# Kernel optimization log

Measured on AMD Instinct MI355X. Metric: run time of the kernel, lower is better.

The kernel has to match this reference:

```python
import jax, jax.numpy as jnp
import numpy as np

B, C, L = 8, 512, 2048
D = C // 8  # qk projection dim


def setup_inputs() -> dict:
    key = jax.random.key(0)
    ks = jax.random.split(key, 7)
    s = 0.02
    return {
        "x": jax.random.normal(ks[0], (B, C, L), dtype=jnp.float32),
        "data_mask": jnp.zeros((B, L, L), dtype=bool),
        "Wq": jax.random.normal(ks[1], (D, C), dtype=jnp.float32) * s,
        "bq": jnp.zeros((D,), dtype=jnp.float32),
        "Wk": jax.random.normal(ks[2], (D, C), dtype=jnp.float32) * s,
        "bk": jnp.zeros((D,), dtype=jnp.float32),
        "Wv": jax.random.normal(ks[3], (C, C), dtype=jnp.float32) * s,
        "bv": jnp.zeros((C,), dtype=jnp.float32),
    }


def reference(x, data_mask, Wq, bq, Wk, bk, Wv, bv):
    # Conv1d(kernel_size=1) == pointwise linear over channel dim.
    Lx = x.shape[-1]
    q = jnp.einsum("dc,bcl->bld", Wq, x) + bq              # (B, L, D)  == query_conv(x).permute(0,2,1)
    k = jnp.einsum("dc,bcl->bdl", Wk, x) + bk[:, None]     # (B, D, L)
    energy = jnp.einsum("bld,bdm->blm", q, k)              # (B, L, L)
    causal = jnp.triu(jnp.ones((Lx, Lx), dtype=bool), k=1)  # strictly-upper = masked
    mask = causal[None, :, :] | data_mask
    energy = jnp.where(mask, -jnp.inf, energy)
    attention = jax.nn.softmax(energy, axis=-1)            # (B, L, L)
    v = jnp.einsum("oc,bcl->bol", Wv, x) + bv[:, None]     # (B, C, L)
    # out = bmm(proj_value, attention^T): out[b,c,m] = sum_l v[b,c,l] * attention[b,m,l]
    out = jnp.einsum("bcl,bml->bcm", v, attention)         # (B, C, L)
    return out, attention
```

## Files before the change

### kernel.cpp

```cpp
#include <hip/hip_runtime.h>
#include <cstddef>
#include <math.h>

#define B_ 8
#define C_ 512
#define L_ 2048
#define D_ 64

typedef __bf16 bf16x8 __attribute__((ext_vector_type(8)));
typedef __bf16 bf16x4 __attribute__((ext_vector_type(4)));
typedef float f32x4 __attribute__((ext_vector_type(4)));

#define MFMA16 __builtin_amdgcn_mfma_f32_16x16x32_bf16

__device__ __forceinline__ void async_lds16(const void* g, void* l) {
  __builtin_amdgcn_global_load_lds(
      (const __attribute__((address_space(1))) void*)g,
      (__attribute__((address_space(3))) void*)l, 16, 0, 0);
}

__global__ __launch_bounds__(256) void transpose_cvt(const float* __restrict__ x,
                                                     __bf16* __restrict__ xT) {
  __shared__ float ts[64][68];
  const int b = blockIdx.z;
  const int l0 = blockIdx.x * 64, c0 = blockIdx.y * 64;
  const int t = threadIdx.x;
  const float* xb = x + ((size_t)b * C_ + c0) * L_ + l0;
#pragma unroll
  for (int kq = 0; kq < 4; ++kq) {
    const int i = t + kq * 256;
    const int row = i >> 4, col4 = i & 15;
    const float4 v = *(const float4*)(xb + (size_t)row * L_ + col4 * 4);
    *(f32x4*)&ts[row][col4 * 4] = *(const f32x4*)&v;
  }
  __syncthreads();
  __bf16* xTb = xT + ((size_t)b * L_ + l0) * C_ + c0;
  const int l = t >> 2, cq = (t & 3) * 16;
  bf16x8 o0, o1;
#pragma unroll
  for (int j = 0; j < 8; ++j) o0[j] = (__bf16)ts[cq + j][l];
#pragma unroll
  for (int j = 0; j < 8; ++j) o1[j] = (__bf16)ts[cq + 8 + j][l];
  *(bf16x8*)(xTb + (size_t)l * C_ + cq) = o0;
  *(bf16x8*)(xTb + (size_t)l * C_ + cq + 8) = o1;
}

__global__ __launch_bounds__(256) void prep_qkv(
    const float* __restrict__ Wq, const float* __restrict__ Wk,
    const float* __restrict__ Wv, const float* __restrict__ bq,
    const float* __restrict__ bk, const float* __restrict__ bv,
    __bf16* __restrict__ W, float* __restrict__ bias) {
  const int i = blockIdx.x * 256 + threadIdx.x;
  const int rq = 64 * 512 / 4;
  const int rk = 128 * 512 / 4;
  const float* src;
  int j;
  if (i < rq) {
    src = Wq; j = i;
  } else if (i < rk) {
    src = Wk; j = i - rq;
  } else {
    src = Wv; j = i - rk;
  }
  float4 v = ((const float4*)src)[j];
  bf16x4 h = {(__bf16)v.x, (__bf16)v.y, (__bf16)v.z, (__bf16)v.w};
  ((bf16x4*)W)[i] = h;
  if (blockIdx.x == 0) {
    for (int t = threadIdx.x; t < 640; t += 256)
      bias[t] = t < 64 ? bq[t] : (t < 128 ? bk[t - 64] : bv[t - 128]);
  }
}

__global__ __launch_bounds__(256) void gemm_qkv(
    const __bf16* __restrict__ A, const __bf16* __restrict__ Bm,
    const float* __restrict__ bias, __bf16* __restrict__ qh,
    __bf16* __restrict__ kh, __bf16* __restrict__ vh) {
  __shared__ __align__(16) __bf16 Ash[128 * 32];
  __shared__ __align__(16) __bf16 Bsh[128 * 32];
  const int b = blockIdx.z;
  const int m0 = blockIdx.x * 128;
  const int n0 = blockIdx.y * 128;
  const int tid = threadIdx.x;
  const int w = tid >> 6, lane = tid & 63;
  const int wm = (w & 1) * 64, wn = (w >> 1) * 64;
  const int lm = lane & 15, q8 = lane >> 4;
  const int srow = lane >> 2;
  const int sk8 = (lane & 3) ^ ((lane >> 3) & 3);

  const __bf16* Bb = Bm + (size_t)b * L_ * C_;
  f32x4 acc[4][4] = {};

  for (int k0 = 0; k0 < C_; k0 += 32) {
#pragma unroll
    for (int t = 0; t < 2; ++t) {
      const int rb = (t * 4 + w) * 16;
      async_lds16(A + (size_t)(m0 + rb + srow) * C_ + k0 + sk8 * 8,
                  &Ash[rb * 32]);
      async_lds16(Bb + (size_t)(n0 + rb + srow) * C_ + k0 + sk8 * 8,
                  &Bsh[rb * 32]);
    }
    __syncthreads();
    const int swz = (q8 ^ ((lm >> 1) & 3)) * 8;
    bf16x8 afr[4], bfr[4];
#pragma unroll
    for (int i = 0; i < 4; ++i) {
      afr[i] = *(const bf16x8*)&Ash[(wm + i * 16 + lm) * 32 + swz];
      bfr[i] = *(const bf16x8*)&Bsh[(wn + i * 16 + lm) * 32 + swz];
    }
#pragma unroll
    for (int i = 0; i < 4; ++i)
#pragma unroll
      for (int j = 0; j < 4; ++j)
        acc[i][j] = MFMA16(afr[i], bfr[j], acc[i][j], 0, 0, 0);
    __syncthreads();
  }

#pragma unroll
  for (int i = 0; i < 4; ++i) {
#pragma unroll
    for (int j = 0; j < 4; ++j) {
      const int ng = n0 + wn + j * 16 + lm;
      const int mg = m0 + wm + i * 16 + q8 * 4;
      if (mg < 128) {
        bf16x4 h;
#pragma unroll
        for (int r = 0; r < 4; ++r) h[r] = (__bf16)(acc[i][j][r] + bias[mg + r]);
        if (mg < 64)
          *(bf16x4*)&qh[((size_t)b * L_ + ng) * 64 + mg] = h;
        else
          *(bf16x4*)&kh[((size_t)b * L_ + ng) * 64 + mg - 64] = h;
      } else {
#pragma unroll
        for (int r = 0; r < 4; ++r)
          vh[((size_t)b * C_ + mg - 128 + r) * L_ + ng] =
              (__bf16)(acc[i][j][r] + bias[mg + r]);
      }
    }
  }
}

__global__ __launch_bounds__(256) void row_sums(
    const __bf16* __restrict__ q, const __bf16* __restrict__ k,
    const unsigned char* __restrict__ mask, float* __restrict__ sinv) {
  __shared__ __align__(16) __bf16 qs[32 * 64];
  __shared__ __align__(16) __bf16 ks[2][128 * 64];
  __shared__ __align__(16) unsigned char msk[2][32 * 128];
  __shared__ float sums[4][32];
  const int b = blockIdx.y;
  const int s = (b < 4) ? (int)blockIdx.x : 63 - (int)blockIdx.x;
  const int r0 = s * 32;
  const int T = (r0 + 31) / 128 + 1;
  const int tid = threadIdx.x;
  const int w = tid >> 6, lane = tid & 63;
  const int lm = lane & 15, q8 = lane >> 4;
  const __bf16* qb = q + (size_t)b * L_ * D_;
  const __bf16* kb = k + (size_t)b * L_ * D_;
  const int krow = lane >> 3;
  const int kk8 = (lane & 7) ^ ((lane >> 3) & 7);

  async_lds16(qb + (size_t)r0 * D_ + tid * 8, &qs[w * 512]);
#pragma unroll
  for (int r = 0; r < 4; ++r)
    async_lds16(kb + (size_t)(r * 32 + w * 8 + krow) * 64 + kk8 * 8,
                &ks[0][(r * 32 + w * 8) * 64]);
  async_lds16(mask + ((size_t)b * L_ + r0 + w * 8 + krow) * L_ + (lane & 7) * 16,
              &msk[0][w * 1024]);

  bf16x8 af[2][2];
  float rsum[2][4] = {};
  for (int t = 0; t < T; ++t) {
    const int t0 = t * 128, buf = t & 1;
    __syncthreads();
    if (t == 0) {
#pragma unroll
      for (int i = 0; i < 2; ++i)
#pragma unroll
        for (int kk = 0; kk < 2; ++kk)
          af[i][kk] = *(const bf16x8*)&qs[(i * 16 + lm) * 64 + kk * 32 + q8 * 8];
    }
    if (t + 1 < T) {
      const int nt0 = t0 + 128, nb = (t + 1) & 1;
#pragma unroll
      for (int r = 0; r < 4; ++r)
        async_lds16(kb + (size_t)(nt0 + r * 32 + w * 8 + krow) * 64 + kk8 * 8,
                    &ks[nb][(r * 32 + w * 8) * 64]);
      async_lds16(mask + ((size_t)b * L_ + r0 + w * 8 + krow) * L_ + nt0 +
                      (lane & 7) * 16,
                  &msk[nb][w * 1024]);
    }
    f32x4 acc[2][2] = {};
#pragma unroll
    for (int kk = 0; kk < 2; ++kk) {
#pragma unroll
      for (int j = 0; j < 2; ++j) {
        const int n = w * 32 + j * 16 + lm;
        const int k8i = kk * 4 + q8;
        bf16x8 bf = *(const bf16x8*)&ks[buf][n * 64 + ((k8i ^ (n & 7)) * 8)];
#pragma unroll
        for (int i = 0; i < 2; ++i)
          acc[i][j] = MFMA16(af[i][kk], bf, acc[i][j], 0, 0, 0);
      }
    }
#pragma unroll
    for (int i = 0; i < 2; ++i)
#pragma unroll
      for (int j = 0; j < 2; ++j)
#pragma unroll
        for (int r = 0; r < 4; ++r) {
          const int lr = i * 16 + q8 * 4 + r;
          const int mcol = w * 32 + j * 16 + lm;
          const int l = r0 + lr, m = t0 + mcol;
          const bool ok = (m <= l) && (msk[buf][lr * 128 + mcol] == 0);
          rsum[i][r] += ok ? __expf(acc[i][j][r]) : 0.f;
        }
  }
#pragma unroll
  for (int i = 0; i < 2; ++i)
#pragma unroll
    for (int r = 0; r < 4; ++r) {
      float vv = rsum[i][r];
      vv += __shfl_xor(vv, 1);
      vv += __shfl_xor(vv, 2);
      vv += __shfl_xor(vv, 4);
      vv += __shfl_xor(vv, 8);
      if (lm == 0) sums[w][i * 16 + q8 * 4 + r] = vv;
    }
  __syncthreads();
  if (tid < 32)
    sinv[(size_t)b * L_ + r0 + tid] =
        1.f / (sums[0][tid] + sums[1][tid] + sums[2][tid] + sums[3][tid]);
}

__global__ __launch_bounds__(256) void attn_fused(
    const __bf16* __restrict__ q, const __bf16* __restrict__ k,
    const __bf16* __restrict__ v, const unsigned char* __restrict__ mask,
    const float* __restrict__ sinv, float* __restrict__ att,
    float* __restrict__ out) {
  __shared__ __align__(16) __bf16 qs[32 * 64];
  __shared__ __align__(16) __bf16 ks[2][128 * 64];
  __shared__ __align__(16) unsigned char msk[2][32 * 128];
  __shared__ __align__(16) __bf16 Ps[32 * 136];
  const int gid = blockIdx.x;
  const int b = gid & 7;
  const int s0 = gid >> 3;
  const int s = (s0 < 32) ? s0 : 95 - s0;
  const int r0 = s * 32;
  const int T = (r0 + 31) / 128 + 1;
  const int tid = threadIdx.x;
  const int w = tid >> 6, lane = tid & 63;
  const int lm = lane & 15, q8 = lane >> 4;
  const __bf16* qb = q + (size_t)b * L_ * D_;
  const __bf16* kb = k + (size_t)b * L_ * D_;
  const __bf16* vb = v + (size_t)b * C_ * L_;
  const int krow = lane >> 3;
  const int kk8 = (lane & 7) ^ ((lane >> 3) & 7);

  float inv[2][4];
#pragma unroll
  for (int i = 0; i < 2; ++i)
#pragma unroll
    for (int r = 0; r < 4; ++r)
      inv[i][r] = sinv[(size_t)b * L_ + r0 + i * 16 + q8 * 4 + r];

  bf16x8 af[2][2];
  f32x4 accO[2][8] = {};

  async_lds16(qb + (size_t)r0 * D_ + tid * 8, &qs[w * 512]);
#pragma unroll
  for (int r = 0; r < 4; ++r)
    async_lds16(kb + (size_t)(r * 32 + w * 8 + krow) * 64 + kk8 * 8,
                &ks[0][(r * 32 + w * 8) * 64]);
  async_lds16(mask + ((size_t)b * L_ + r0 + w * 8 + krow) * L_ + (lane & 7) * 16,
              &msk[0][w * 1024]);

  for (int t = 0; t < T; ++t) {
    const int t0 = t * 128, buf = t & 1;
    __syncthreads();
    if (t == 0) {
#pragma unroll
      for (int i = 0; i < 2; ++i)
#pragma unroll
        for (int kk = 0; kk < 2; ++kk)
          af[i][kk] = *(const bf16x8*)&qs[(i * 16 + lm) * 64 + kk * 32 + q8 * 8];
    }
    if (t + 1 < T) {
      const int nt0 = t0 + 128, nb = (t + 1) & 1;
#pragma unroll
      for (int r = 0; r < 4; ++r)
        async_lds16(kb + (size_t)(nt0 + r * 32 + w * 8 + krow) * 64 + kk8 * 8,
                    &ks[nb][(r * 32 + w * 8) * 64]);
      async_lds16(mask + ((size_t)b * L_ + r0 + w * 8 + krow) * L_ + nt0 +
                      (lane & 7) * 16,
                  &msk[nb][w * 1024]);
    }
    f32x4 acc[2][2] = {};
#pragma unroll
    for (int kk = 0; kk < 2; ++kk) {
#pragma unroll
      for (int j = 0; j < 2; ++j) {
        const int n = w * 32 + j * 16 + lm;
        const int k8i = kk * 4 + q8;
        bf16x8 bf = *(const bf16x8*)&ks[buf][n * 64 + ((k8i ^ (n & 7)) * 8)];
#pragma unroll
        for (int i = 0; i < 2; ++i)
          acc[i][j] = MFMA16(af[i][kk], bf, acc[i][j], 0, 0, 0);
      }
    }
#pragma unroll
    for (int i = 0; i < 2; ++i)
#pragma unroll
      for (int j = 0; j < 2; ++j)
#pragma unroll
        for (int r = 0; r < 4; ++r) {
          const int lr = i * 16 + q8 * 4 + r;
          const int mcol = w * 32 + j * 16 + lm;
          const int l = r0 + lr, m = t0 + mcol;
          const bool ok = (m <= l) && (msk[buf][lr * 128 + mcol] == 0);
          const float p = ok ? __expf(acc[i][j][r]) : 0.f;
          att[((size_t)b * L_ + l) * L_ + m] = p * inv[i][r];
          Ps[lr * 136 + mcol] = (__bf16)p;
        }
    asm volatile("s_waitcnt lgkmcnt(0)\n\ts_barrier" ::: "memory");
    __builtin_amdgcn_sched_barrier(0);
#pragma unroll
    for (int kk = 0; kk < 4; ++kk) {
      bf16x8 pa[2];
#pragma unroll
      for (int i = 0; i < 2; ++i)
        pa[i] = *(const bf16x8*)&Ps[(i * 16 + lm) * 136 + kk * 32 + q8 * 8];
#pragma unroll
      for (int cf = 0; cf < 8; ++cf) {
        const int c = w * 128 + cf * 16 + lm;
        bf16x8 bv =
            *(const bf16x8*)(vb + (size_t)c * L_ + t0 + kk * 32 + q8 * 8);
#pragma unroll
        for (int i = 0; i < 2; ++i)
          accO[i][cf] = MFMA16(pa[i], bv, accO[i][cf], 0, 0, 0);
      }
    }
  }

#pragma unroll
  for (int i = 0; i < 2; ++i)
#pragma unroll
    for (int cf = 0; cf < 8; ++cf) {
      const int c = w * 128 + cf * 16 + lm;
      f32x4 o;
      o[0] = accO[i][cf][0] * inv[i][0];
      o[1] = accO[i][cf][1] * inv[i][1];
      o[2] = accO[i][cf][2] * inv[i][2];
      o[3] = accO[i][cf][3] * inv[i][3];
      *(f32x4*)(out + ((size_t)b * C_ + c) * L_ + r0 + i * 16 + q8 * 4) = o;
    }

  const f32x4 z4 = {0.f, 0.f, 0.f, 0.f};
  for (int rr = 0; rr < 32; ++rr) {
    float* arow = att + ((size_t)b * L_ + r0 + rr) * L_;
    for (int c = T * 128 + tid * 4; c < L_; c += 1024) *(f32x4*)&arow[c] = z4;
  }
}

extern "C" void kernel_launch(void* const* d_in, const int* in_sizes, int n_in,
                              void* d_out, int out_size, void* d_ws,
                              size_t ws_size, hipStream_t stream) {
  const float* x = (const float*)d_in[0];
  const unsigned char* dmask = (const unsigned char*)d_in[1];
  const float* Wq = (const float*)d_in[2];
  const float* bq = (const float*)d_in[3];
  const float* Wk = (const float*)d_in[4];
  const float* bk = (const float*)d_in[5];
  const float* Wv = (const float*)d_in[6];
  const float* bv = (const float*)d_in[7];

  float* out = (float*)d_out;
  float* att = out + (size_t)B_ * C_ * L_;

  __bf16* qh = (__bf16*)d_ws;
  __bf16* kh = qh + (size_t)B_ * L_ * D_;
  __bf16* xTh = kh + (size_t)B_ * L_ * D_;
  __bf16* vh = xTh + (size_t)B_ * L_ * C_;
  __bf16* Wqkv = vh + (size_t)B_ * C_ * L_;
  float* bqkv = (float*)(Wqkv + (size_t)640 * C_);
  float* sinv = (float*)xTh;

  dim3 blk(256);
  transpose_cvt<<<dim3(L_ / 64, C_ / 64, B_), blk, 0, stream>>>(x, xTh);
  prep_qkv<<<dim3(320), blk, 0, stream>>>(Wq, Wk, Wv, bq, bk, bv, Wqkv, bqkv);
  gemm_qkv<<<dim3(5, L_ / 128, B_), blk, 0, stream>>>(Wqkv, xTh, bqkv, qh, kh,
                                                      vh);
  row_sums<<<dim3(64, B_), blk, 0, stream>>>(qh, kh, dmask, sinv);
  attn_fused<<<dim3(512), blk, 0, stream>>>(qh, kh, vh, dmask, sinv, att, out);
}
```

Before: 406.9 us.

## Double-buffer QKV GEMM LDS loads and remap grids for XCD locality

The QKV projection GEMM now double-buffers its shared-memory tiles, issuing async loads for the next K-slice before computing on the current one. Each iteration ends with a single explicit waitcnt plus barrier instead of two syncthreads. Both gemm_qkv and row_sums move to 1D grids whose block index is decoded so that blocks sharing a batch land on the same XCD. In row_sums the causal workload is balanced by pairing short and long row strips. The costs are twice the LDS footprint in the GEMM and hand-written synchronisation that must stay correct.

```diff
diff --git a/kernel.cpp b/kernel.cpp
--- a/kernel.cpp
+++ b/kernel.cpp
@@ -75,11 +75,16 @@
     const __bf16* __restrict__ A, const __bf16* __restrict__ Bm,
     const float* __restrict__ bias, __bf16* __restrict__ qh,
     __bf16* __restrict__ kh, __bf16* __restrict__ vh) {
-  __shared__ __align__(16) __bf16 Ash[128 * 32];
-  __shared__ __align__(16) __bf16 Bsh[128 * 32];
-  const int b = blockIdx.z;
-  const int m0 = blockIdx.x * 128;
-  const int n0 = blockIdx.y * 128;
+  __shared__ __align__(16) __bf16 Ash[2][128 * 32];
+  __shared__ __align__(16) __bf16 Bsh[2][128 * 32];
+  const int bid = blockIdx.x;
+  const int xcd = bid & 7;
+  const int inner = bid >> 3;
+  const int m_i = inner % 5;
+  const int g = xcd + 8 * (inner / 5);
+  const int m0 = m_i * 128;
+  const int n0 = (g & 15) * 128;
+  const int b = g >> 4;
   const int tid = threadIdx.x;
   const int w = tid >> 6, lane = tid & 63;
   const int wm = (w & 1) * 64, wn = (w >> 1) * 64;
@@ -90,29 +95,37 @@
   const __bf16* Bb = Bm + (size_t)b * L_ * C_;
   f32x4 acc[4][4] = {};
 
-  for (int k0 = 0; k0 < C_; k0 += 32) {
+  auto stage = [&](int bf, int k0) {
 #pragma unroll
     for (int t = 0; t < 2; ++t) {
       const int rb = (t * 4 + w) * 16;
       async_lds16(A + (size_t)(m0 + rb + srow) * C_ + k0 + sk8 * 8,
-                  &Ash[rb * 32]);
+                  &Ash[bf][rb * 32]);
       async_lds16(Bb + (size_t)(n0 + rb + srow) * C_ + k0 + sk8 * 8,
-                  &Bsh[rb * 32]);
-    }
-    __syncthreads();
+                  &Bsh[bf][rb * 32]);
+    }
+  };
+
+  stage(0, 0);
+  __syncthreads();
+
+  for (int s = 0; s < 16; ++s) {
+    const int buf = s & 1;
+    if (s + 1 < 16) stage(buf ^ 1, (s + 1) * 32);
     const int swz = (q8 ^ ((lm >> 1) & 3)) * 8;
     bf16x8 afr[4], bfr[4];
 #pragma unroll
     for (int i = 0; i < 4; ++i) {
-      afr[i] = *(const bf16x8*)&Ash[(wm + i * 16 + lm) * 32 + swz];
-      bfr[i] = *(const bf16x8*)&Bsh[(wn + i * 16 + lm) * 32 + swz];
+      afr[i] = *(const bf16x8*)&Ash[buf][(wm + i * 16 + lm) * 32 + swz];
+      bfr[i] = *(const bf16x8*)&Bsh[buf][(wn + i * 16 + lm) * 32 + swz];
     }
 #pragma unroll
     for (int i = 0; i < 4; ++i)
 #pragma unroll
       for (int j = 0; j < 4; ++j)
         acc[i][j] = MFMA16(afr[i], bfr[j], acc[i][j], 0, 0, 0);
-    __syncthreads();
+    asm volatile("s_waitcnt vmcnt(0) lgkmcnt(0)\n\ts_barrier" ::: "memory");
+    __builtin_amdgcn_sched_barrier(0);
   }
 
 #pragma unroll
@@ -146,8 +159,10 @@
   __shared__ __align__(16) __bf16 ks[2][128 * 64];
   __shared__ __align__(16) unsigned char msk[2][32 * 128];
   __shared__ float sums[4][32];
-  const int b = blockIdx.y;
-  const int s = (b < 4) ? (int)blockIdx.x : 63 - (int)blockIdx.x;
+  const int gid = blockIdx.x;
+  const int b = gid & 7;
+  const int s0 = gid >> 3;
+  const int s = (s0 < 32) ? s0 : 95 - s0;
   const int r0 = s * 32;
   const int T = (r0 + 31) / 128 + 1;
   const int tid = threadIdx.x;
@@ -386,8 +401,7 @@
   dim3 blk(256);
   transpose_cvt<<<dim3(L_ / 64, C_ / 64, B_), blk, 0, stream>>>(x, xTh);
   prep_qkv<<<dim3(320), blk, 0, stream>>>(Wq, Wk, Wv, bq, bk, bv, Wqkv, bqkv);
-  gemm_qkv<<<dim3(5, L_ / 128, B_), blk, 0, stream>>>(Wqkv, xTh, bqkv, qh, kh,
-                                                      vh);
-  row_sums<<<dim3(64, B_), blk, 0, stream>>>(qh, kh, dmask, sinv);
+  gemm_qkv<<<dim3(640), blk, 0, stream>>>(Wqkv, xTh, bqkv, qh, kh, vh);
+  row_sums<<<dim3(512), blk, 0, stream>>>(qh, kh, dmask, sinv);
   attn_fused<<<dim3(512), blk, 0, stream>>>(qh, kh, vh, dmask, sinv, att, out);
 }
```

Measured after the change: 408.7 us. No clear change (+0.4%).
